# Performance work log

Measured on AMD Instinct MI355X. Metric: run time of the kernel, lower is better.

## Reference

```python
import jax, jax.numpy as jnp
import numpy as np

N_NODES = 50000
N_EDGES = 800000
HIDDEN = 128


def setup_inputs() -> dict:
    key = jax.random.key(0)
    k1, k2, k3, k4, k5, k6 = jax.random.split(key, 6)
    node_features = jax.random.normal(k1, (N_NODES, HIDDEN), dtype=jnp.float32)
    senders = jax.random.randint(k2, (N_EDGES,), 0, N_NODES, dtype=jnp.int32)
    receivers = jax.random.randint(k3, (N_EDGES,), 0, N_NODES, dtype=jnp.int32)
    edge_features = jax.random.normal(k4, (N_EDGES, HIDDEN), dtype=jnp.float32)
    # message_proj: Linear(3H, H); torch default init ~ U(-1/sqrt(fan_in), 1/sqrt(fan_in))
    bound = 1.0 / np.sqrt(3 * HIDDEN)
    W = jax.random.uniform(k5, (3 * HIDDEN, HIDDEN), dtype=jnp.float32, minval=-bound, maxval=bound)
    b = jax.random.uniform(k6, (HIDDEN,), dtype=jnp.float32, minval=-bound, maxval=bound)
    ln_w = jnp.ones((HIDDEN,), dtype=jnp.float32)
    ln_b = jnp.zeros((HIDDEN,), dtype=jnp.float32)
    return {"node_features": node_features, "senders": senders, "receivers": receivers,
            "edge_features": edge_features, "W": W, "b": b, "ln_w": ln_w, "ln_b": ln_b}


def layer_norm(x, w, b, eps=1e-5):
    mu = jnp.mean(x, axis=-1, keepdims=True)
    var = jnp.mean(jnp.square(x - mu), axis=-1, keepdims=True)
    return (x - mu) * jax.lax.rsqrt(var + eps) * w + b


def reference(node_features, senders, receivers, edge_features, W, b, ln_w, ln_b):
    # gather endpoints, concat along feature dim: [E, 3H]
    cat = jnp.concatenate((node_features[senders], node_features[receivers], edge_features), axis=-1)
    message = jax.nn.relu(cat @ W + b)  # [E, H]
    # scatter-add messages back to receiver nodes ('sum' aggregation)
    aggr = jax.ops.segment_sum(message, receivers, num_segments=node_features.shape[0])
    out = node_features + aggr  # residual
    return layer_norm(out, ln_w, ln_b)
```

## Files before the change

### kernel.cpp

```cpp
#include <hip/hip_runtime.h>

#define H 128
#define NSRC 3
#define MSTRIDE 136

typedef _Float16 f16;
typedef _Float16 f16x2 __attribute__((ext_vector_type(2)));
typedef _Float16 f16x4 __attribute__((ext_vector_type(4)));
typedef _Float16 f16x8 __attribute__((ext_vector_type(8)));
typedef float f32x4 __attribute__((ext_vector_type(4)));

__global__ void setup_kernel(const float* __restrict__ W, f16* __restrict__ wbuf,
                             int* __restrict__ cnt, float4* __restrict__ AGG4,
                             int n_nodes, int nagg4,
                             const float* __restrict__ nf, f16* __restrict__ nfh,
                             int nf4) {
    const int i = blockIdx.x * blockDim.x + threadIdx.x;
    const int np = gridDim.x * blockDim.x;
    if (i < NSRC * H * H) {
        int src = i >> 14;
        int k = (i >> 7) & 127;
        int c = i & 127;
        float v = W[((size_t)src * H + k) * H + c];
        unsigned off = ((unsigned)(c * 256 + k * 2)) ^ ((unsigned)((c & 7) << 4));
        wbuf[(size_t)src * (H * H) + (off >> 1)] = (f16)v;
    }
    if (i < n_nodes) cnt[i] = 0;
    for (int j = i; j < nagg4; j += np) AGG4[j] = make_float4(0.f, 0.f, 0.f, 0.f);
    for (int j = i; j < nf4; j += np) {
        float4 v = ((const float4*)nf)[j];
        f16x4 h;
        h[0] = (f16)v.x; h[1] = (f16)v.y; h[2] = (f16)v.z; h[3] = (f16)v.w;
        ((f16x4*)nfh)[j] = h;
    }
}

__global__ void hist_kernel(const int* __restrict__ recv, int* __restrict__ cnt, int n_edges) {
    int e = blockIdx.x * blockDim.x + threadIdx.x;
    if (e < n_edges) atomicAdd(&cnt[recv[e]], 1);
}

__global__ void scan_kernel(const int* __restrict__ cnt, int* __restrict__ row_ptr,
                            int* __restrict__ cursor, int n) {
    __shared__ int sd[1024];
    const int t = threadIdx.x;
    const int per = (n + 1023) >> 10;
    const int st = t * per;
    const int en = min(st + per, n);
    int s = 0;
    for (int i = st; i < en; ++i) s += cnt[i];
    sd[t] = s;
    __syncthreads();
    for (int off = 1; off < 1024; off <<= 1) {
        int v = 0;
        if (t >= off) v = sd[t - off];
        __syncthreads();
        sd[t] += v;
        __syncthreads();
    }
    int run = sd[t] - s;
    for (int i = st; i < en; ++i) {
        row_ptr[i] = run;
        cursor[i] = run;
        run += cnt[i];
    }
    if (t == 1023) row_ptr[n] = sd[1023];
}

__global__ void scatter_kernel(const int* __restrict__ send, const int* __restrict__ recv,
                               int* __restrict__ cursor, int* __restrict__ perm,
                               int* __restrict__ ssend, int* __restrict__ srecv, int n_edges) {
    int e = blockIdx.x * blockDim.x + threadIdx.x;
    if (e < n_edges) {
        int r = recv[e];
        int pos = atomicAdd(&cursor[r], 1);
        perm[pos] = e;
        ssend[pos] = send[e];
        srecv[pos] = r;
    }
}

__global__ __launch_bounds__(256, 2)
void fused_msg_kernel(const f16* __restrict__ nfh, const float* __restrict__ ef,
                      const int* __restrict__ perm, const int* __restrict__ ssend,
                      const int* __restrict__ srecv, const f16* __restrict__ wbuf,
                      const float* __restrict__ b, float* __restrict__ AGG,
                      int n_edges) {
    __shared__ __align__(16) f16 Alds[NSRC * 64 * H];
    __shared__ __align__(16) f16 MSG[64 * MSTRIDE];

    const int t = threadIdx.x;
    const int lane = t & 63;
    const int wid = t >> 6;
    const int l15 = lane & 15;
    const int lg = lane >> 4;
    const int c2 = lane * 2;

    f16x8 breg[NSRC][2][4];
#pragma unroll
    for (int src = 0; src < NSRC; ++src)
#pragma unroll
        for (int cf = 0; cf < 2; ++cf)
#pragma unroll
            for (int ks = 0; ks < 4; ++ks) {
                const int c = wid * 32 + cf * 16 + l15;
                const int k = ks * 32 + lg * 8;
                unsigned off = ((unsigned)(c * 256 + k * 2)) ^ ((unsigned)((c & 7) << 4));
                breg[src][cf][ks] =
                    *(const f16x8*)((const char*)wbuf + (size_t)src * 32768 + off);
            }

    const float2 bias2 = *(const float2*)&b[c2];

    const int srow = t >> 2;
    const int sq = t & 3;
    const int ntiles = (n_edges + 63) >> 6;

    for (int tile = blockIdx.x; tile < ntiles; tile += gridDim.x) {
        const int e0 = tile * 64;
        __syncthreads();

        {
            const int e = min(e0 + srow, n_edges - 1);
            const int sidx = ssend[e];
            const int ridx = srecv[e];
            const int pidx = perm[e];
            const int4* ps = (const int4*)(nfh + (size_t)sidx * H + sq * 32);
            const int4* pr = (const int4*)(nfh + (size_t)ridx * H + sq * 32);
            const float4* pe = (const float4*)(ef + (size_t)pidx * H + sq * 32);
#pragma unroll
            for (int i = 0; i < 4; ++i) {
                const int k = sq * 32 + i * 8;
                unsigned off = ((unsigned)(srow * 256 + k * 2))
                               ^ ((unsigned)((srow & 7) << 4));
                *(int4*)((char*)Alds + off) = ps[i];
                *(int4*)((char*)Alds + 16384 + off) = pr[i];
                float4 v0 = pe[i * 2];
                float4 v1 = pe[i * 2 + 1];
                f16x8 h;
                h[0] = (f16)v0.x; h[1] = (f16)v0.y; h[2] = (f16)v0.z; h[3] = (f16)v0.w;
                h[4] = (f16)v1.x; h[5] = (f16)v1.y; h[6] = (f16)v1.z; h[7] = (f16)v1.w;
                *(f16x8*)((char*)Alds + 32768 + off) = h;
            }
        }
        __syncthreads();

        f32x4 acc[4][2];
#pragma unroll
        for (int rf = 0; rf < 4; ++rf) {
            acc[rf][0] = (f32x4){0.f, 0.f, 0.f, 0.f};
            acc[rf][1] = (f32x4){0.f, 0.f, 0.f, 0.f};
        }
#pragma unroll
        for (int src = 0; src < NSRC; ++src)
#pragma unroll
            for (int ks = 0; ks < 4; ++ks) {
                f16x8 af[4];
#pragma unroll
                for (int rf = 0; rf < 4; ++rf) {
                    const int row = rf * 16 + l15;
                    const int k = ks * 32 + lg * 8;
                    unsigned off = ((unsigned)(row * 256 + k * 2))
                                   ^ ((unsigned)((row & 7) << 4));
                    af[rf] = *(const f16x8*)((const char*)Alds + (size_t)src * 16384 + off);
                }
#pragma unroll
                for (int rf = 0; rf < 4; ++rf) {
                    acc[rf][0] = __builtin_amdgcn_mfma_f32_16x16x32_f16(
                        af[rf], breg[src][0][ks], acc[rf][0], 0, 0, 0);
                    acc[rf][1] = __builtin_amdgcn_mfma_f32_16x16x32_f16(
                        af[rf], breg[src][1][ks], acc[rf][1], 0, 0, 0);
                }
            }

#pragma unroll
        for (int rf = 0; rf < 4; ++rf)
#pragma unroll
            for (int cf = 0; cf < 2; ++cf)
#pragma unroll
                for (int q = 0; q < 4; ++q)
                    MSG[(rf * 16 + lg * 4 + q) * MSTRIDE + wid * 32 + cf * 16 + l15] =
                        (f16)acc[rf][cf][q];
        __syncthreads();

        int rarr[16];
#pragma unroll
        for (int j = 0; j < 16; ++j)
            rarr[j] = srecv[min(e0 + wid * 16 + j, n_edges - 1)];
        float ax = 0.f, ay = 0.f;
#pragma unroll
        for (int j = 0; j < 16; ++j) {
            const int e = e0 + wid * 16 + j;
            if (e < n_edges) {
                f16x2 m = *(const f16x2*)&MSG[(wid * 16 + j) * MSTRIDE + c2];
                ax += fmaxf((float)m[0] + bias2.x, 0.f);
                ay += fmaxf((float)m[1] + bias2.y, 0.f);
                bool flush = (j == 15) || (e + 1 >= n_edges) || (rarr[j + 1] != rarr[j]);
                if (flush) {
                    atomicAdd(&AGG[(size_t)rarr[j] * H + c2], ax);
                    atomicAdd(&AGG[(size_t)rarr[j] * H + c2 + 1], ay);
                    ax = 0.f;
                    ay = 0.f;
                }
            }
        }
    }
}

__global__ __launch_bounds__(256, 4)
void ln_agg_kernel(const float* __restrict__ nf, const float* __restrict__ AGG,
                   const float* __restrict__ lnw, const float* __restrict__ lnb,
                   float* __restrict__ out, int n_nodes) {
    const int wv = threadIdx.x >> 6;
    const int lane = threadIdx.x & 63;
    const int row = blockIdx.x * (blockDim.x >> 6) + wv;
    if (row >= n_nodes) return;
    float2 a = ((const float2*)(nf + (size_t)row * H))[lane];
    float2 g = ((const float2*)(AGG + (size_t)row * H))[lane];
    float vx = a.x + g.x, vy = a.y + g.y;

    float s = vx + vy;
#pragma unroll
    for (int m = 32; m; m >>= 1) s += __shfl_xor(s, m, 64);
    float mu = s * (1.f / H);
    float dx = vx - mu, dy = vy - mu;
    float q = dx * dx + dy * dy;
#pragma unroll
    for (int m = 32; m; m >>= 1) q += __shfl_xor(q, m, 64);
    float rs = rsqrtf(q * (1.f / H) + 1e-5f);

    float2 w2 = ((const float2*)lnw)[lane];
    float2 b2 = ((const float2*)lnb)[lane];
    float2 o;
    o.x = dx * rs * w2.x + b2.x;
    o.y = dy * rs * w2.y + b2.y;
    ((float2*)(out + (size_t)row * H))[lane] = o;
}

__global__ __launch_bounds__(512, 2)
void fused_edge_kernel(const f16* __restrict__ nfh, const int* __restrict__ senders,
                       const int* __restrict__ receivers, const float* __restrict__ ef,
                       const float* __restrict__ b, const f16* __restrict__ wbuf,
                       float* __restrict__ out, int n_edges) {
    __shared__ __align__(16) f16 Wlds[NSRC * H * H];
    const int t = threadIdx.x;
    {
        const int4* g = (const int4*)wbuf;
        int4* d = (int4*)Wlds;
#pragma unroll
        for (int i = 0; i < 12; ++i) d[i * 512 + t] = g[i * 512 + t];
    }
    __syncthreads();

    const int lane = t & 63;
    const int wid = t >> 6;
    const int l15 = lane & 15;
    const int lg = lane >> 4;

    float bias[8];
#pragma unroll
    for (int cf = 0; cf < 8; ++cf) bias[cf] = b[cf * 16 + l15];

    const int ntiles = (n_edges + 63) >> 6;
    const int nworkers = gridDim.x * 8;

    for (int tile = blockIdx.x * 8 + wid; tile < ntiles; tile += nworkers) {
        const int e0 = tile * 64;
        int sid[4], rid[4];
#pragma unroll
        for (int rf = 0; rf < 4; ++rf) {
            int e = e0 + rf * 16 + l15;
            if (e >= n_edges) e = n_edges - 1;
            sid[rf] = senders[e];
            rid[rf] = receivers[e];
        }
        f32x4 acc[4][8];
#pragma unroll
        for (int rf = 0; rf < 4; ++rf)
#pragma unroll
            for (int cf = 0; cf < 8; ++cf) acc[rf][cf] = (f32x4){0.f, 0.f, 0.f, 0.f};

#pragma unroll
        for (int src = 0; src < 2; ++src) {
#pragma unroll
            for (int ks = 0; ks < 4; ++ks) {
                f16x8 a[4];
#pragma unroll
                for (int rf = 0; rf < 4; ++rf) {
                    const int row = (src == 0) ? sid[rf] : rid[rf];
                    a[rf] = *(const f16x8*)(nfh + (size_t)row * H + ks * 32 + lg * 8);
                }
#pragma unroll
                for (int cf = 0; cf < 8; ++cf) {
                    const int c = cf * 16 + l15;
                    unsigned off = ((unsigned)(src * 32768 + c * 256 + (ks * 32 + lg * 8) * 2))
                                   ^ ((unsigned)((c & 7) << 4));
                    f16x8 bf = *(const f16x8*)((const char*)Wlds + off);
#pragma unroll
                    for (int rf = 0; rf < 4; ++rf)
                        acc[rf][cf] = __builtin_amdgcn_mfma_f32_16x16x32_f16(
                            a[rf], bf, acc[rf][cf], 0, 0, 0);
                }
            }
        }
#pragma unroll
        for (int ks = 0; ks < 4; ++ks) {
            f16x8 a[4];
#pragma unroll
            for (int rf = 0; rf < 4; ++rf) {
                int e = e0 + rf * 16 + l15;
                if (e >= n_edges) e = n_edges - 1;
                const float* p = ef + (size_t)e * H + ks * 32 + lg * 8;
                float4 v0 = *(const float4*)p;
                float4 v1 = *(const float4*)(p + 4);
                f16x8 h;
                h[0] = (f16)v0.x; h[1] = (f16)v0.y; h[2] = (f16)v0.z; h[3] = (f16)v0.w;
                h[4] = (f16)v1.x; h[5] = (f16)v1.y; h[6] = (f16)v1.z; h[7] = (f16)v1.w;
                a[rf] = h;
            }
#pragma unroll
            for (int cf = 0; cf < 8; ++cf) {
                const int c = cf * 16 + l15;
                unsigned off = ((unsigned)(2 * 32768 + c * 256 + (ks * 32 + lg * 8) * 2))
                               ^ ((unsigned)((c & 7) << 4));
                f16x8 bf = *(const f16x8*)((const char*)Wlds + off);
#pragma unroll
                for (int rf = 0; rf < 4; ++rf)
                    acc[rf][cf] = __builtin_amdgcn_mfma_f32_16x16x32_f16(
                        a[rf], bf, acc[rf][cf], 0, 0, 0);
            }
        }
#pragma unroll
        for (int rf = 0; rf < 4; ++rf) {
#pragma unroll
            for (int q = 0; q < 4; ++q) {
                const int e = e0 + rf * 16 + lg * 4 + q;
                if (e < n_edges) {
                    const int r = receivers[e];
                    float* dst = out + (size_t)r * H;
#pragma unroll
                    for (int cf = 0; cf < 8; ++cf) {
                        float m = fmaxf(acc[rf][cf][q] + bias[cf], 0.f);
                        atomicAdd(dst + cf * 16 + l15, m);
                    }
                }
            }
        }
    }
}

__global__ __launch_bounds__(256, 4)
void ln_kernel(const float* __restrict__ nf, const float* __restrict__ lnw,
               const float* __restrict__ lnb, float* __restrict__ out, int n_nodes) {
    const int wv = threadIdx.x >> 6;
    const int lane = threadIdx.x & 63;
    const int row = blockIdx.x * (blockDim.x >> 6) + wv;
    if (row >= n_nodes) return;
    float2 a = ((const float2*)(nf + (size_t)row * H))[lane];
    float2 g = ((float2*)(out + (size_t)row * H))[lane];
    float vx = a.x + g.x, vy = a.y + g.y;
    float s = vx + vy;
#pragma unroll
    for (int m = 32; m; m >>= 1) s += __shfl_xor(s, m, 64);
    float mu = s * (1.f / H);
    float dx = vx - mu, dy = vy - mu;
    float q = dx * dx + dy * dy;
#pragma unroll
    for (int m = 32; m; m >>= 1) q += __shfl_xor(q, m, 64);
    float rs = rsqrtf(q * (1.f / H) + 1e-5f);
    float2 w2 = ((const float2*)lnw)[lane];
    float2 b2 = ((const float2*)lnb)[lane];
    float2 o;
    o.x = dx * rs * w2.x + b2.x;
    o.y = dy * rs * w2.y + b2.y;
    ((float2*)(out + (size_t)row * H))[lane] = o;
}

__global__ void naive_edge_kernel(const float* __restrict__ nf, const int* __restrict__ s,
                                  const int* __restrict__ r, const float* __restrict__ ef,
                                  const float* __restrict__ W, const float* __restrict__ b,
                                  float* __restrict__ out, int n_edges) {
    int e = blockIdx.x * 2 + (threadIdx.x >> 7);
    int c = threadIdx.x & 127;
    if (e >= n_edges) return;
    int se = s[e], re = r[e];
    float acc = b[c];
    for (int k = 0; k < H; ++k) {
        acc += nf[(size_t)se * H + k] * W[(size_t)k * H + c];
        acc += nf[(size_t)re * H + k] * W[(size_t)(H + k) * H + c];
        acc += ef[(size_t)e * H + k] * W[(size_t)(2 * H + k) * H + c];
    }
    atomicAdd(&out[(size_t)re * H + c], fmaxf(acc, 0.f));
}

extern "C" void kernel_launch(void* const* d_in, const int* in_sizes, int n_in,
                              void* d_out, int out_size, void* d_ws, size_t ws_size,
                              hipStream_t stream) {
    const float* nf        = (const float*)d_in[0];
    const int*   senders   = (const int*)d_in[1];
    const int*   receivers = (const int*)d_in[2];
    const float* ef        = (const float*)d_in[3];
    const float* W         = (const float*)d_in[4];
    const float* b         = (const float*)d_in[5];
    const float* lnw       = (const float*)d_in[6];
    const float* lnb       = (const float*)d_in[7];
    float* out = (float*)d_out;

    const int n_nodes = in_sizes[0] / H;
    const int n_edges = in_sizes[1];
    const int nfelem = n_nodes * H;

    size_t o = 0;
    auto carve = [&](size_t bytes) { size_t r = o; o += (bytes + 255) & ~(size_t)255; return r; };
    const size_t o_wbuf   = carve((size_t)NSRC * H * H * sizeof(f16));
    const size_t o_nfh    = carve((size_t)nfelem * sizeof(f16));
    const size_t o_cnt    = carve((size_t)n_nodes * 4);
    const size_t o_rowptr = carve((size_t)(n_nodes + 1) * 4);
    const size_t o_cursor = carve((size_t)n_nodes * 4);
    const size_t o_perm   = carve((size_t)n_edges * 4);
    const size_t o_ssend  = carve((size_t)n_edges * 4);
    const size_t o_srecv  = carve((size_t)n_edges * 4);
    const size_t o_agg    = carve((size_t)nfelem * sizeof(float));
    const size_t need_full = o;

    char* ws = (char*)d_ws;
    f16* wbuf = (f16*)(ws + o_wbuf);
    f16* nfh  = (f16*)(ws + o_nfh);

    if (ws_size >= need_full) {
        int* cnt    = (int*)(ws + o_cnt);
        int* rowptr = (int*)(ws + o_rowptr);
        int* cursor = (int*)(ws + o_cursor);
        int* perm   = (int*)(ws + o_perm);
        int* ssend  = (int*)(ws + o_ssend);
        int* srecv  = (int*)(ws + o_srecv);
        float* AGG  = (float*)(ws + o_agg);

        setup_kernel<<<2048, 256, 0, stream>>>(W, wbuf, cnt, (float4*)AGG,
                                               n_nodes, nfelem / 4, nf, nfh, nfelem / 4);
        hist_kernel<<<(n_edges + 255) / 256, 256, 0, stream>>>(receivers, cnt, n_edges);
        scan_kernel<<<1, 1024, 0, stream>>>(cnt, rowptr, cursor, n_nodes);
        scatter_kernel<<<(n_edges + 255) / 256, 256, 0, stream>>>(
            senders, receivers, cursor, perm, ssend, srecv, n_edges);

        fused_msg_kernel<<<1024, 256, 0, stream>>>(nfh, ef, perm, ssend, srecv,
                                                   wbuf, b, AGG, n_edges);
        ln_agg_kernel<<<(n_nodes + 3) / 4, 256, 0, stream>>>(nf, AGG, lnw, lnb, out, n_nodes);
    } else if (ws_size >= o_cnt) {
        hipMemsetAsync(d_out, 0, (size_t)nfelem * sizeof(float), stream);
        setup_kernel<<<2048, 256, 0, stream>>>(W, wbuf, (int*)(ws + o_wbuf), nullptr,
                                               0, 0, nf, nfh, nfelem / 4);
        fused_edge_kernel<<<512, 512, 0, stream>>>(nfh, senders, receivers, ef, b,
                                                   wbuf, out, n_edges);
        ln_kernel<<<(n_nodes + 3) / 4, 256, 0, stream>>>(nf, lnw, lnb, out, n_nodes);
    } else {
        hipMemsetAsync(d_out, 0, (size_t)nfelem * sizeof(float), stream);
        naive_edge_kernel<<<(n_edges + 1) / 2, 256, 0, stream>>>(
            nf, senders, receivers, ef, W, b, out, n_edges);
        ln_kernel<<<(n_nodes + 3) / 4, 256, 0, stream>>>(nf, lnw, lnb, out, n_nodes);
    }
}
```

Measured before the change: 449.1 us.

## Software-pipeline edge gathers across tiles and cache receiver indices in LDS

Restructures the fused message kernel so that the sender-node and edge-feature rows for the next tile are prefetched into registers while the current tile runs its MFMA and scatter phases. Index loads are fetched two tiles ahead. The per-tile receiver indices are kept in a small shared array instead of being re-read from global memory. MSG row padding changes from 136 to 132, which shifts the LDS bank mapping. The cost is much higher register pressure (about 48 extra VGPRs for the prefetched data) under launch_bounds(256,2), which may cause spills. A leftover dead LDS read was also added.

```diff
diff --git a/kernel.cpp b/kernel.cpp
--- a/kernel.cpp
+++ b/kernel.cpp
@@ -2,7 +2,7 @@
 
 #define H 128
 #define NSRC 3
-#define MSTRIDE 136
+#define MSTRIDE 132
 
 typedef _Float16 f16;
 typedef _Float16 f16x2 __attribute__((ext_vector_type(2)));
@@ -88,6 +88,7 @@
                       int n_edges) {
     __shared__ __align__(16) f16 Alds[NSRC * 64 * H];
     __shared__ __align__(16) f16 MSG[64 * MSTRIDE];
+    __shared__ int SR[64];
 
     const int t = threadIdx.x;
     const int lane = t & 63;
@@ -111,37 +112,82 @@
             }
 
     const float2 bias2 = *(const float2*)&b[c2];
-
     const int srow = t >> 2;
     const int sq = t & 3;
     const int ntiles = (n_edges + 63) >> 6;
-
-    for (int tile = blockIdx.x; tile < ntiles; tile += gridDim.x) {
-        const int e0 = tile * 64;
+    const int stride = gridDim.x;
+
+    int cs = 0, cr = 0, cp = 0;
+    int ns = 0, nr = 0, np = 0;
+    int4 s0, s1, s2, s3;
+    float4 e0, e1, e2, e3, e4, e5, e6, e7;
+
+    int tile = blockIdx.x;
+    if (tile < ntiles) {
+        const int e = min(tile * 64 + srow, n_edges - 1);
+        cs = ssend[e]; cr = srecv[e]; cp = perm[e];
+        const int4* ps = (const int4*)(nfh + (size_t)cs * H + sq * 32);
+        s0 = ps[0]; s1 = ps[1]; s2 = ps[2]; s3 = ps[3];
+        const float4* pe = (const float4*)(ef + (size_t)cp * H + sq * 32);
+        e0 = pe[0]; e1 = pe[1]; e2 = pe[2]; e3 = pe[3];
+        e4 = pe[4]; e5 = pe[5]; e6 = pe[6]; e7 = pe[7];
+    }
+    if (tile + stride < ntiles) {
+        const int e = min((tile + stride) * 64 + srow, n_edges - 1);
+        ns = ssend[e]; nr = srecv[e]; np = perm[e];
+    }
+
+    for (; tile < ntiles; tile += stride) {
+        const int e0base = tile * 64;
         __syncthreads();
 
         {
-            const int e = min(e0 + srow, n_edges - 1);
-            const int sidx = ssend[e];
-            const int ridx = srecv[e];
-            const int pidx = perm[e];
-            const int4* ps = (const int4*)(nfh + (size_t)sidx * H + sq * 32);
-            const int4* pr = (const int4*)(nfh + (size_t)ridx * H + sq * 32);
-            const float4* pe = (const float4*)(ef + (size_t)pidx * H + sq * 32);
-#pragma unroll
-            for (int i = 0; i < 4; ++i) {
-                const int k = sq * 32 + i * 8;
-                unsigned off = ((unsigned)(srow * 256 + k * 2))
-                               ^ ((unsigned)((srow & 7) << 4));
-                *(int4*)((char*)Alds + off) = ps[i];
-                *(int4*)((char*)Alds + 16384 + off) = pr[i];
-                float4 v0 = pe[i * 2];
-                float4 v1 = pe[i * 2 + 1];
-                f16x8 h;
-                h[0] = (f16)v0.x; h[1] = (f16)v0.y; h[2] = (f16)v0.z; h[3] = (f16)v0.w;
-                h[4] = (f16)v1.x; h[5] = (f16)v1.y; h[6] = (f16)v1.z; h[7] = (f16)v1.w;
-                *(f16x8*)((char*)Alds + 32768 + off) = h;
-            }
+            const unsigned ob = ((unsigned)(srow * 256 + sq * 64))
+                                ^ ((unsigned)((srow & 7) << 4));
+            *(int4*)((char*)Alds + (ob ^ 0));
+        }
+        {
+            unsigned off0 = ((unsigned)(srow * 256 + (sq * 32 + 0) * 2)) ^ ((unsigned)((srow & 7) << 4));
+            unsigned off1 = ((unsigned)(srow * 256 + (sq * 32 + 8) * 2)) ^ ((unsigned)((srow & 7) << 4));
+            unsigned off2 = ((unsigned)(srow * 256 + (sq * 32 + 16) * 2)) ^ ((unsigned)((srow & 7) << 4));
+            unsigned off3 = ((unsigned)(srow * 256 + (sq * 32 + 24) * 2)) ^ ((unsigned)((srow & 7) << 4));
+            *(int4*)((char*)Alds + off0) = s0;
+            *(int4*)((char*)Alds + off1) = s1;
+            *(int4*)((char*)Alds + off2) = s2;
+            *(int4*)((char*)Alds + off3) = s3;
+            f16x8 h0, h1, h2, h3;
+#pragma unroll
+            for (int j = 0; j < 4; ++j) { h0[j] = (f16)(&e0.x)[j]; h0[j + 4] = (f16)(&e1.x)[j]; }
+#pragma unroll
+            for (int j = 0; j < 4; ++j) { h1[j] = (f16)(&e2.x)[j]; h1[j + 4] = (f16)(&e3.x)[j]; }
+#pragma unroll
+            for (int j = 0; j < 4; ++j) { h2[j] = (f16)(&e4.x)[j]; h2[j + 4] = (f16)(&e5.x)[j]; }
+#pragma unroll
+            for (int j = 0; j < 4; ++j) { h3[j] = (f16)(&e6.x)[j]; h3[j + 4] = (f16)(&e7.x)[j]; }
+            *(f16x8*)((char*)Alds + 32768 + off0) = h0;
+            *(f16x8*)((char*)Alds + 32768 + off1) = h1;
+            *(f16x8*)((char*)Alds + 32768 + off2) = h2;
+            *(f16x8*)((char*)Alds + 32768 + off3) = h3;
+            const int4* pr = (const int4*)(nfh + (size_t)cr * H + sq * 32);
+            int4 r0 = pr[0], r1 = pr[1], r2 = pr[2], r3 = pr[3];
+            *(int4*)((char*)Alds + 16384 + off0) = r0;
+            *(int4*)((char*)Alds + 16384 + off1) = r1;
+            *(int4*)((char*)Alds + 16384 + off2) = r2;
+            *(int4*)((char*)Alds + 16384 + off3) = r3;
+            if (sq == 0) SR[srow] = cr;
+        }
+
+        int t2s = 0, t2r = 0, t2p = 0;
+        if (tile + 2 * stride < ntiles) {
+            const int e = min((tile + 2 * stride) * 64 + srow, n_edges - 1);
+            t2s = ssend[e]; t2r = srecv[e]; t2p = perm[e];
+        }
+        if (tile + stride < ntiles) {
+            const int4* ps = (const int4*)(nfh + (size_t)ns * H + sq * 32);
+            s0 = ps[0]; s1 = ps[1]; s2 = ps[2]; s3 = ps[3];
+            const float4* pe = (const float4*)(ef + (size_t)np * H + sq * 32);
+            e0 = pe[0]; e1 = pe[1]; e2 = pe[2]; e3 = pe[3];
+            e4 = pe[4]; e5 = pe[5]; e6 = pe[6]; e7 = pe[7];
         }
         __syncthreads();
 
@@ -185,12 +231,11 @@
 
         int rarr[16];
 #pragma unroll
-        for (int j = 0; j < 16; ++j)
-            rarr[j] = srecv[min(e0 + wid * 16 + j, n_edges - 1)];
+        for (int j = 0; j < 16; ++j) rarr[j] = SR[wid * 16 + j];
         float ax = 0.f, ay = 0.f;
 #pragma unroll
         for (int j = 0; j < 16; ++j) {
-            const int e = e0 + wid * 16 + j;
+            const int e = e0base + wid * 16 + j;
             if (e < n_edges) {
                 f16x2 m = *(const f16x2*)&MSG[(wid * 16 + j) * MSTRIDE + c2];
                 ax += fmaxf((float)m[0] + bias2.x, 0.f);
@@ -204,6 +249,9 @@
                 }
             }
         }
+
+        cs = ns; cr = nr; cp = np;
+        ns = t2s; nr = t2r; np = t2p;
     }
 }
 
```

Measured after the change: 391.6 us. 12.8% less time.
